# Optimization experiments

Measured on AMD Instinct MI355X. Metric: run time of the kernel, lower is better.

Reference implementation:

```python
import jax, jax.numpy as jnp
import numpy as np

EMB = 1024
N_HEAD = 16
HEAD = 64
D_FF = 4 * EMB
LN_EPS = 1e-5


def layernorm(x, g, b):
    mu = jnp.mean(x, axis=-1, keepdims=True)
    var = jnp.mean(jnp.square(x - mu), axis=-1, keepdims=True)
    return (x - mu) * jax.lax.rsqrt(var + LN_EPS) * g + b


def setup_inputs() -> dict:
    key = jax.random.key(0)
    ks = jax.random.split(key, 12)
    s = 0.02
    x = jax.random.normal(ks[0], (4, 2048, EMB), dtype=jnp.float32)
    # per-head Q/K/V projections (no bias), stacked along head axis
    Wq = jax.random.normal(ks[1], (N_HEAD, EMB, HEAD), dtype=jnp.float32) * s
    Wk = jax.random.normal(ks[2], (N_HEAD, EMB, HEAD), dtype=jnp.float32) * s
    Wv = jax.random.normal(ks[3], (N_HEAD, EMB, HEAD), dtype=jnp.float32) * s
    Wo = jax.random.normal(ks[4], (EMB, EMB), dtype=jnp.float32) * s
    bo = jnp.zeros((EMB,), dtype=jnp.float32)
    ln1_g = jnp.ones((EMB,), dtype=jnp.float32)
    ln1_b = jnp.zeros((EMB,), dtype=jnp.float32)
    W1 = jax.random.normal(ks[5], (EMB, D_FF), dtype=jnp.float32) * s
    b1 = jnp.zeros((D_FF,), dtype=jnp.float32)
    W2 = jax.random.normal(ks[6], (D_FF, EMB), dtype=jnp.float32) * s
    b2 = jnp.zeros((EMB,), dtype=jnp.float32)
    ln2_g = jnp.ones((EMB,), dtype=jnp.float32)
    ln2_b = jnp.zeros((EMB,), dtype=jnp.float32)
    return dict(x=x, Wq=Wq, Wk=Wk, Wv=Wv, Wo=Wo, bo=bo, ln1_g=ln1_g,
                ln1_b=ln1_b, W1=W1, b1=b1, W2=W2, b2=b2, ln2_g=ln2_g,
                ln2_b=ln2_b)


def reference(x, Wq, Wk, Wv, Wo, bo, ln1_g, ln1_b, W1, b1, W2, b2, ln2_g, ln2_b):
    B, T, _ = x.shape
    # fused multi-head QKV (equivalent to the per-head Python loop + concat)
    q = jnp.einsum('btd,hdk->bhtk', x, Wq)
    k = jnp.einsum('btd,hdk->bhtk', x, Wk)
    v = jnp.einsum('btd,hdk->bhtk', x, Wv)
    scores = jnp.einsum('bhtk,bhsk->bhts', q, k) / jnp.sqrt(jnp.float32(HEAD))
    att = jax.nn.softmax(scores, axis=-1)
    heads = jnp.einsum('bhts,bhsk->bhtk', att, v)           # [B,H,T,head]
    cat = heads.transpose(0, 2, 1, 3).reshape(B, T, EMB)     # concat over heads
    mha = cat @ Wo + bo
    x = x + layernorm(mha, ln1_g, ln1_b)                     # residual of LN(sublayer)
    ff = jax.nn.gelu(x @ W1 + b1, approximate=False) @ W2 + b2
    x = x + layernorm(ff, ln2_g, ln2_b)
    return x
```

## Files before the change

### kernel.cpp

```cpp
#include <hip/hip_runtime.h>
#include <math.h>


using u16 = unsigned short;
typedef __bf16 bf16x8 __attribute__((ext_vector_type(8)));
typedef __bf16 bf16x4 __attribute__((ext_vector_type(4)));
typedef unsigned short u16x8 __attribute__((ext_vector_type(8)));
typedef unsigned short u16x4 __attribute__((ext_vector_type(4)));
typedef float f32x4 __attribute__((ext_vector_type(4)));

#if defined(__has_builtin)
#if __has_builtin(__builtin_amdgcn_exp2f)
#define EXP2F(x) __builtin_amdgcn_exp2f(x)
#endif
#endif
#ifndef EXP2F
#define EXP2F(x) __expf((x) * 0.69314718055994531f)
#endif

__device__ __forceinline__ float bf2f(u16 h) {
  return __uint_as_float(((unsigned int)h) << 16);
}
__device__ __forceinline__ u16 f2bf(float f) {
  unsigned int u = __float_as_uint(f);
  u += 0x7fffu + ((u >> 16) & 1u);
  return (u16)(u >> 16);
}

__device__ __forceinline__ void gload_lds16(const void* g, void* l) {
  __builtin_amdgcn_global_load_lds(
      (__attribute__((address_space(1))) void*)(g),
      (__attribute__((address_space(3))) void*)(l), 16, 0, 0);
}

__global__ __launch_bounds__(256) void detect_dtype(const u16* __restrict__ x,
                                                    int* __restrict__ flag) {
  __shared__ int cnt[256];
  int c = 0;
#pragma unroll
  for (int j = 0; j < 8; ++j) {
    float v = bf2f(x[threadIdx.x * 8 + j]);
    float a = fabsf(v);
    if (a >= 1e-4f && a <= 64.0f) ++c;
  }
  cnt[threadIdx.x] = c;
  __syncthreads();
  if (threadIdx.x == 0) {
    int t = 0;
    for (int i = 0; i < 256; ++i) t += cnt[i];
    flag[0] = (t < 1638) ? 1 : 0;
  }
}

__global__ __launch_bounds__(256) void cvt_copy(const void* __restrict__ in,
                                                u16* __restrict__ out,
                                                const int* __restrict__ flagp,
                                                long n) {
  long idx = ((long)blockIdx.x * 256 + threadIdx.x) * 4;
  if (idx >= n) return;
  if (*flagp) {
    float4 v = *(const float4*)((const float*)in + idx);
    out[idx] = f2bf(v.x); out[idx + 1] = f2bf(v.y);
    out[idx + 2] = f2bf(v.z); out[idx + 3] = f2bf(v.w);
  } else {
    *(u16x4*)(out + idx) = *(const u16x4*)((const u16*)in + idx);
  }
}

__global__ __launch_bounds__(256) void cvt_vecs(
    const void* s0, const void* s1, const void* s2, const void* s3,
    const void* s4, const void* s5, const void* s6, u16* __restrict__ dst,
    const int* __restrict__ flagp) {
  const int lens[7] = {1024, 1024, 1024, 4096, 1024, 1024, 1024};
  const int offs[7] = {0, 1024, 2048, 3072, 7168, 8192, 9216};
  const void* srcs[7] = {s0, s1, s2, s3, s4, s5, s6};
  int w = blockIdx.x;
  int f = *flagp;
  for (int i = threadIdx.x; i < lens[w]; i += 256)
    dst[offs[w] + i] = f ? f2bf(((const float*)srcs[w])[i])
                         : ((const u16*)srcs[w])[i];
}

__global__ __launch_bounds__(256) void transpose_cvt(
    const void* __restrict__ in, u16* __restrict__ out, int R, int C,
    long inBS, long outBS, const int* __restrict__ flagp) {
  __shared__ u16 tile[32][33];
  int f = *flagp;
  u16* ob = out + (long)blockIdx.z * outBS;
  int c = blockIdx.x * 32 + threadIdx.x;
  int r0 = blockIdx.y * 32;
  if (f) {
    const float* ib = (const float*)in + (long)blockIdx.z * inBS;
#pragma unroll
    for (int i = threadIdx.y; i < 32; i += 8)
      tile[i][threadIdx.x] = f2bf(ib[(long)(r0 + i) * C + c]);
  } else {
    const u16* ib = (const u16*)in + (long)blockIdx.z * inBS;
#pragma unroll
    for (int i = threadIdx.y; i < 32; i += 8)
      tile[i][threadIdx.x] = ib[(long)(r0 + i) * C + c];
  }
  __syncthreads();
  int r = r0 + threadIdx.x;
  int c0 = blockIdx.x * 32;
#pragma unroll
  for (int i = threadIdx.y; i < 32; i += 8)
    ob[(long)(c0 + i) * R + r] = tile[threadIdx.x][i];
}

__global__ __launch_bounds__(256) void kv_frag(const u16* __restrict__ qkv,
                                               u16* __restrict__ KF,
                                               u16* __restrict__ VF) {
  __shared__ u16 Kt[64][72];
  __shared__ u16 Vt[64][72];
  const int jblk = blockIdx.x, bh = blockIdx.y;
  const int b = bh >> 4, h = bh & 15;
  const int tid = threadIdx.x;
  const long j0 = jblk * 64;

  {
    int tt = tid >> 2, c0 = (tid & 3) * 16;
    const u16* src = qkv + (long)(b * 2048 + j0 + tt) * 3072 + h * 64 + c0;
    *(u16x8*)(&Kt[tt][c0]) = *(const u16x8*)(src + 1024);
    *(u16x8*)(&Kt[tt][c0 + 8]) = *(const u16x8*)(src + 1024 + 8);
    *(u16x8*)(&Vt[tt][c0]) = *(const u16x8*)(src + 2048);
    *(u16x8*)(&Vt[tt][c0 + 8]) = *(const u16x8*)(src + 2048 + 8);
  }
  __syncthreads();

  long obase = ((long)bh * 32 + jblk) * 8 * 512;
#pragma unroll
  for (int si = 0; si < 2; ++si) {
    int s = tid * 2 + si;
    int f = s >> 6, ln = s & 63;
    int kt = f >> 2, nt = f & 3;
    int lr = ln & 15, lq = ln >> 4;
    u16x8 ko, vo;
#pragma unroll
    for (int j = 0; j < 8; ++j) {
      ko[j] = Kt[nt * 16 + lr][kt * 32 + lq * 8 + j];
      vo[j] = Vt[kt * 32 + lq * 8 + j][nt * 16 + lr];
    }
    *(u16x8*)(KF + obase + (long)s * 8) = ko;
    *(u16x8*)(VF + obase + (long)s * 8) = vo;
  }
}

__device__ __forceinline__ bf16x8 fragld64(const u16* lb, int row, int ks,
                                           int lq) {
  int slot = ((ks << 2) | lq) ^ (row & 7);
  return *(const bf16x8*)(lb + row * 64 + slot * 8);
}

template <int EPI, int BN>
__global__ __launch_bounds__(512, 2) void gemm2ph(
    const u16* __restrict__ A, const u16* __restrict__ Bt,
    const u16* __restrict__ bias, u16* __restrict__ Cout,
    int M, int N, int K) {
  static_assert(BN == 256 || BN == 128, "");
  constexpr int NFQ = BN / 128;
  __shared__ u16 As[2][16384];
  __shared__ u16 Bs[2][BN * 64];
  const int tid = threadIdx.x;
  const int wave = tid >> 6, lane = tid & 63;
  const int lr = lane & 15, lq = lane >> 4;

  const int MT = M >> 8, NTt = N / BN;
  const int nwg = MT * NTt;
  int wg = blockIdx.x;
  if (!(nwg & 7)) wg = (wg & 7) * (nwg >> 3) + (wg >> 3);
  const int tm = wg % MT, tn = wg / MT;
  const long m0 = (long)tm << 8;
  const long n0 = (long)tn * BN;

  const int wm = (wave >> 2) << 7;
  const int wn = (wave & 3) * (BN / 4);

  const int srow = lane >> 3;
  const int skoff = ((lane & 7) ^ srow) * 8;

  auto stage = [&](int buf, int t) {
#pragma unroll
    for (int j = 0; j < 4; ++j)
      gload_lds16(
          A + (m0 + j * 64 + wave * 8 + srow) * (long)K + t * 64 + skoff,
          &As[buf][j * 4096 + (wave << 9)]);
#pragma unroll
    for (int j = 0; j < BN / 64; ++j)
      gload_lds16(
          Bt + (n0 + j * 64 + wave * 8 + srow) * (long)K + t * 64 + skoff,
          &Bs[buf][j * 4096 + (wave << 9)]);
  };

  f32x4 acc[8][2 * NFQ] = {};
  const int NT = K >> 6;
  int cur = 0;

  stage(0, 0);
  __syncthreads();

  for (int t = 0; t < NT; ++t) {
    const u16* Ab = As[cur];
    const u16* Bb = Bs[cur];
    if (t + 1 < NT) stage(cur ^ 1, t + 1);

    bf16x8 a_[4][2], b0_[NFQ][2], b1_[NFQ][2];
#pragma unroll
    for (int mf = 0; mf < 4; ++mf)
#pragma unroll
      for (int ks = 0; ks < 2; ++ks)
        a_[mf][ks] = fragld64(Ab, wm + mf * 16 + lr, ks, lq);
#pragma unroll
    for (int nf = 0; nf < NFQ; ++nf)
#pragma unroll
      for (int ks = 0; ks < 2; ++ks)
        b0_[nf][ks] = fragld64(Bb, wn + nf * 16 + lr, ks, lq);
#pragma unroll
    for (int mf = 0; mf < 4; ++mf)
#pragma unroll
      for (int nf = 0; nf < NFQ; ++nf)
#pragma unroll
        for (int ks = 0; ks < 2; ++ks)
          acc[mf][nf] = __builtin_amdgcn_mfma_f32_16x16x32_bf16(
              a_[mf][ks], b0_[nf][ks], acc[mf][nf], 0, 0, 0);
#pragma unroll
    for (int nf = 0; nf < NFQ; ++nf)
#pragma unroll
      for (int ks = 0; ks < 2; ++ks)
        b1_[nf][ks] = fragld64(Bb, wn + BN / 8 + nf * 16 + lr, ks, lq);
#pragma unroll
    for (int mf = 0; mf < 4; ++mf)
#pragma unroll
      for (int nf = 0; nf < NFQ; ++nf)
#pragma unroll
        for (int ks = 0; ks < 2; ++ks)
          acc[mf][NFQ + nf] = __builtin_amdgcn_mfma_f32_16x16x32_bf16(
              a_[mf][ks], b1_[nf][ks], acc[mf][NFQ + nf], 0, 0, 0);
#pragma unroll
    for (int mf = 0; mf < 4; ++mf)
#pragma unroll
      for (int ks = 0; ks < 2; ++ks)
        a_[mf][ks] = fragld64(Ab, wm + 64 + mf * 16 + lr, ks, lq);
#pragma unroll
    for (int mf = 0; mf < 4; ++mf)
#pragma unroll
      for (int nf = 0; nf < NFQ; ++nf)
#pragma unroll
        for (int ks = 0; ks < 2; ++ks)
          acc[4 + mf][NFQ + nf] = __builtin_amdgcn_mfma_f32_16x16x32_bf16(
              a_[mf][ks], b1_[nf][ks], acc[4 + mf][NFQ + nf], 0, 0, 0);
#pragma unroll
    for (int mf = 0; mf < 4; ++mf)
#pragma unroll
      for (int nf = 0; nf < NFQ; ++nf)
#pragma unroll
        for (int ks = 0; ks < 2; ++ks)
          acc[4 + mf][nf] = __builtin_amdgcn_mfma_f32_16x16x32_bf16(
              a_[mf][ks], b0_[nf][ks], acc[4 + mf][nf], 0, 0, 0);

    __syncthreads();
    cur ^= 1;
  }

  const int rq = lq * 4;
#pragma unroll
  for (int mf = 0; mf < 8; ++mf)
#pragma unroll
    for (int nf2 = 0; nf2 < 2 * NFQ; ++nf2) {
      const int col = (int)n0 + wn + nf2 * 16 + lr;
#pragma unroll
      for (int r = 0; r < 4; ++r) {
        const long row = m0 + wm + mf * 16 + rq + r;
        float v = acc[mf][nf2][r];
        if (EPI == 2) {
          v += bf2f(bias[col]);
          v = 0.5f * v * (1.0f + erff(v * 0.70710678118654752f));
        } else if (EPI == 3) {
          v += bf2f(bias[col]);
        }
        Cout[row * (long)N + col] = f2bf(v);
      }
    }
}

template <int EPI>
__global__ __launch_bounds__(512, 2) void gemm3buf(
    const u16* __restrict__ A, const u16* __restrict__ Bt,
    const u16* __restrict__ bias, u16* __restrict__ Cout,
    int M, int N, int K) {
  __shared__ u16 As[3][16384];
  __shared__ u16 Bs[3][8192];
  const int tid = threadIdx.x;
  const int wave = tid >> 6, lane = tid & 63;
  const int lr = lane & 15, lq = lane >> 4;

  const int MT = M >> 8, NTt = N >> 7;
  const int nwg = MT * NTt;
  int wg = blockIdx.x;
  if (!(nwg & 7)) wg = (wg & 7) * (nwg >> 3) + (wg >> 3);
  const int tm = wg % MT, tn = wg / MT;
  const long m0 = (long)tm << 8;
  const long n0 = (long)tn << 7;

  const int wm = (wave >> 2) << 7;
  const int wn = (wave & 3) * 32;

  const int srow = lane >> 3;
  const int skoff = ((lane & 7) ^ srow) * 8;

  auto stage = [&](u16* ab, u16* bb, int t) {
#pragma unroll
    for (int j = 0; j < 4; ++j)
      gload_lds16(
          A + (m0 + j * 64 + wave * 8 + srow) * (long)K + t * 64 + skoff,
          ab + j * 4096 + (wave << 9));
#pragma unroll
    for (int j = 0; j < 2; ++j)
      gload_lds16(
          Bt + (n0 + j * 64 + wave * 8 + srow) * (long)K + t * 64 + skoff,
          bb + j * 4096 + (wave << 9));
  };

  u16 *pa0 = &As[0][0], *pa1 = &As[1][0], *pa2 = &As[2][0];
  u16 *pb0 = &Bs[0][0], *pb1 = &Bs[1][0], *pb2 = &Bs[2][0];

  f32x4 acc[8][2] = {};
  const int NT = K >> 6;

  stage(pa0, pb0, 0);
  stage(pa1, pb1, 1);
  asm volatile("s_waitcnt vmcnt(6)" ::: "memory");
  __builtin_amdgcn_s_barrier();
  __builtin_amdgcn_sched_barrier(0);

  for (int t = 0; t < NT; ++t) {
    const bool pf = (t + 2 < NT);
    if (pf) stage(pa2, pb2, t + 2);

    bf16x8 a_[4][2], b0_[2], b1_[2];
#pragma unroll
    for (int mf = 0; mf < 4; ++mf)
#pragma unroll
      for (int ks = 0; ks < 2; ++ks)
        a_[mf][ks] = fragld64(pa0, wm + mf * 16 + lr, ks, lq);
#pragma unroll
    for (int ks = 0; ks < 2; ++ks) b0_[ks] = fragld64(pb0, wn + lr, ks, lq);
#pragma unroll
    for (int mf = 0; mf < 4; ++mf)
#pragma unroll
      for (int ks = 0; ks < 2; ++ks)
        acc[mf][0] = __builtin_amdgcn_mfma_f32_16x16x32_bf16(
            a_[mf][ks], b0_[ks], acc[mf][0], 0, 0, 0);
#pragma unroll
    for (int ks = 0; ks < 2; ++ks)
      b1_[ks] = fragld64(pb0, wn + 16 + lr, ks, lq);
#pragma unroll
    for (int mf = 0; mf < 4; ++mf)
#pragma unroll
      for (int ks = 0; ks < 2; ++ks)
        acc[mf][1] = __builtin_amdgcn_mfma_f32_16x16x32_bf16(
            a_[mf][ks], b1_[ks], acc[mf][1], 0, 0, 0);
#pragma unroll
    for (int mf = 0; mf < 4; ++mf)
#pragma unroll
      for (int ks = 0; ks < 2; ++ks)
        a_[mf][ks] = fragld64(pa0, wm + 64 + mf * 16 + lr, ks, lq);
#pragma unroll
    for (int mf = 0; mf < 4; ++mf)
#pragma unroll
      for (int ks = 0; ks < 2; ++ks)
        acc[4 + mf][1] = __builtin_amdgcn_mfma_f32_16x16x32_bf16(
            a_[mf][ks], b1_[ks], acc[4 + mf][1], 0, 0, 0);
#pragma unroll
    for (int mf = 0; mf < 4; ++mf)
#pragma unroll
      for (int ks = 0; ks < 2; ++ks)
        acc[4 + mf][0] = __builtin_amdgcn_mfma_f32_16x16x32_bf16(
            a_[mf][ks], b0_[ks], acc[4 + mf][0], 0, 0, 0);

    if (pf)
      asm volatile("s_waitcnt vmcnt(6) lgkmcnt(0)" ::: "memory");
    else
      asm volatile("s_waitcnt vmcnt(0) lgkmcnt(0)" ::: "memory");
    __builtin_amdgcn_s_barrier();
    __builtin_amdgcn_sched_barrier(0);

    u16* ta = pa0; pa0 = pa1; pa1 = pa2; pa2 = ta;
    u16* tb = pb0; pb0 = pb1; pb1 = pb2; pb2 = tb;
  }

  const int rq = lq * 4;
#pragma unroll
  for (int mf = 0; mf < 8; ++mf)
#pragma unroll
    for (int nf2 = 0; nf2 < 2; ++nf2) {
      const int col = (int)n0 + wn + nf2 * 16 + lr;
#pragma unroll
      for (int r = 0; r < 4; ++r) {
        const long row = m0 + wm + mf * 16 + rq + r;
        float v = acc[mf][nf2][r];
        if (EPI == 2) {
          v += bf2f(bias[col]);
          v = 0.5f * v * (1.0f + erff(v * 0.70710678118654752f));
        } else if (EPI == 3) {
          v += bf2f(bias[col]);
        }
        Cout[row * (long)N + col] = f2bf(v);
      }
    }
}

__global__ __launch_bounds__(256, 3) void flash_attn(
    const u16* __restrict__ qkv, const u16* __restrict__ KF,
    const u16* __restrict__ VF, u16* __restrict__ cat) {
  const int T = 2048, LD = 3072;
  const float QSCALE = 0.18033688011112042f;
  const float EXPC = 4.3280851226677321f;
  const int bh = blockIdx.y;
  const int b = bh >> 4, h = bh & 15;
  const int tid = threadIdx.x, wave = tid >> 6, lane = tid & 63;
  const int lr = lane & 15, lq = lane >> 4;

  __shared__ u16 Ps[4 * 32 * 64];
  u16* Pw = Ps + wave * 32 * 64;

  const u16* Qb = qkv + (long)(b * 2048) * LD + h * 64;
  const long fbase = (long)bh * 32 * 8 * 512;

  bf16x8 aq[2][2];
#pragma unroll
  for (int st = 0; st < 2; ++st) {
    int qrow = blockIdx.x * 128 + wave * 32 + st * 16 + lr;
#pragma unroll
    for (int kt = 0; kt < 2; ++kt) {
      u16x8 q = *(const u16x8*)(Qb + (long)qrow * LD + kt * 32 + lq * 8);
      bf16x8 t;
#pragma unroll
      for (int j = 0; j < 8; ++j) t[j] = (__bf16)(bf2f(q[j]) * QSCALE);
      aq[st][kt] = t;
    }
  }

  f32x4 o[2][4] = {};
  float lsum[2] = {0.0f, 0.0f};

  for (int jblk = 0; jblk < T / 64; ++jblk) {
    const u16* kf = KF + fbase + (long)jblk * 8 * 512;
    const u16* vf = VF + fbase + (long)jblk * 8 * 512;

    bf16x8 bk[2][4];
#pragma unroll
    for (int kt = 0; kt < 2; ++kt)
#pragma unroll
      for (int nt = 0; nt < 4; ++nt)
        bk[kt][nt] = *(const bf16x8*)(kf + (kt * 4 + nt) * 512 + lane * 8);

    f32x4 s[2][4] = {};
    __builtin_amdgcn_s_setprio(1);
#pragma unroll
    for (int st = 0; st < 2; ++st)
#pragma unroll
      for (int nt = 0; nt < 4; ++nt)
#pragma unroll
        for (int kt = 0; kt < 2; ++kt)
          s[st][nt] = __builtin_amdgcn_mfma_f32_16x16x32_bf16(
              bk[kt][nt], aq[st][kt], s[st][nt], 0, 0, 0);
    __builtin_amdgcn_s_setprio(0);

    bf16x8 bv[2][4];
#pragma unroll
    for (int kt = 0; kt < 2; ++kt)
#pragma unroll
      for (int nt = 0; nt < 4; ++nt)
        bv[kt][nt] = *(const bf16x8*)(vf + (kt * 4 + nt) * 512 + lane * 8);

#pragma unroll
    for (int st = 0; st < 2; ++st)
#pragma unroll
      for (int nt = 0; nt < 4; ++nt) {
        f32x4 p;
#pragma unroll
        for (int r = 0; r < 4; ++r) p[r] = EXP2F(s[st][nt][r] - EXPC);
        lsum[st] += (p[0] + p[1]) + (p[2] + p[3]);
        bf16x4 pk;
#pragma unroll
        for (int r = 0; r < 4; ++r) pk[r] = (__bf16)p[r];
        int wph = (nt * 2 + (lq >> 1)) ^ (lr & 7);
        *(bf16x4*)(Pw + (st * 16 + lr) * 64 + wph * 8 + (lq & 1) * 4) = pk;
      }

#pragma unroll
    for (int st = 0; st < 2; ++st)
#pragma unroll
      for (int kt = 0; kt < 2; ++kt) {
        bf16x8 ap = *(const bf16x8*)(
            Pw + (st * 16 + lr) * 64 + (((kt * 4 + lq) ^ (lr & 7)) * 8));
        __builtin_amdgcn_s_setprio(1);
#pragma unroll
        for (int nt = 0; nt < 4; ++nt)
          o[st][nt] = __builtin_amdgcn_mfma_f32_16x16x32_bf16(
              ap, bv[kt][nt], o[st][nt], 0, 0, 0);
        __builtin_amdgcn_s_setprio(0);
      }
  }

#pragma unroll
  for (int st = 0; st < 2; ++st) {
    lsum[st] += __shfl_xor(lsum[st], 16, 64);
    lsum[st] += __shfl_xor(lsum[st], 32, 64);
  }

  u16* ob = cat + (long)(b * 2048) * 1024 + h * 64;
#pragma unroll
  for (int st = 0; st < 2; ++st) {
    int trow = blockIdx.x * 128 + wave * 32 + st * 16 + lq * 4;
#pragma unroll
    for (int r = 0; r < 4; ++r) {
      float linv = 1.0f / __shfl(lsum[st], lq * 4 + r, 64);
#pragma unroll
      for (int nt = 0; nt < 4; ++nt)
        ob[(long)(trow + r) * 1024 + nt * 16 + lr] = f2bf(o[st][nt][r] * linv);
    }
  }
}

__global__ __launch_bounds__(256) void ln_residual(
    const u16* __restrict__ y, const void* __restrict__ res, int res_raw,
    const u16* __restrict__ g, const u16* __restrict__ bb,
    void* __restrict__ out, const int* __restrict__ flagp, int final_out) {
  const long row = blockIdx.x;
  const int tid = threadIdx.x, wave = tid >> 6, lane = tid & 63;
  u16x4 yv = *(const u16x4*)(y + row * 1024 + tid * 4);
  float yy[4];
#pragma unroll
  for (int j = 0; j < 4; ++j) yy[j] = bf2f(yv[j]);
  float s1 = yy[0] + yy[1] + yy[2] + yy[3];
  float s2 = yy[0] * yy[0] + yy[1] * yy[1] + yy[2] * yy[2] + yy[3] * yy[3];
#pragma unroll
  for (int off = 1; off < 64; off <<= 1) {
    s1 += __shfl_xor(s1, off, 64);
    s2 += __shfl_xor(s2, off, 64);
  }
  __shared__ float ws1[4], ws2[4];
  if (lane == 0) { ws1[wave] = s1; ws2[wave] = s2; }
  __syncthreads();
  float t1 = ws1[0] + ws1[1] + ws1[2] + ws1[3];
  float t2 = ws2[0] + ws2[1] + ws2[2] + ws2[3];
  float mu = t1 * (1.0f / 1024.0f);
  float var = t2 * (1.0f / 1024.0f) - mu * mu;
  float rstd = rsqrtf(var + 1e-5f);
  int i = tid * 4;
  bool f32in = res_raw && (*flagp);
  bool f32out = final_out && (*flagp);
#pragma unroll
  for (int j = 0; j < 4; ++j) {
    float rv = f32in ? ((const float*)res)[row * 1024 + i + j]
                     : bf2f(((const u16*)res)[row * 1024 + i + j]);
    float o = rv + (yy[j] - mu) * rstd * bf2f(g[i + j]) + bf2f(bb[i + j]);
    if (f32out)
      ((float*)out)[row * 1024 + i + j] = o;
    else
      ((u16*)out)[row * 1024 + i + j] = f2bf(o);
  }
}

extern "C" void kernel_launch(void* const* d_in, const int* in_sizes, int n_in,
                              void* d_out, int out_size, void* d_ws,
                              size_t ws_size, hipStream_t stream) {
  const void* x_raw = d_in[0];
  const void* Wq = d_in[1];
  const void* Wk = d_in[2];
  const void* Wv = d_in[3];
  const void* Wo = d_in[4];
  const void* bo = d_in[5];
  const void* ln1g = d_in[6];
  const void* ln1b = d_in[7];
  const void* W1 = d_in[8];
  const void* b1 = d_in[9];
  const void* W2 = d_in[10];
  const void* b2 = d_in[11];
  const void* ln2g = d_in[12];
  const void* ln2b = d_in[13];

  char* ws = (char*)d_ws;
  u16* qkv = (u16*)(ws + 0);
  u16* mha = (u16*)(ws + 0);
  u16* h1 = (u16*)(ws + 0);
  u16* cat = (u16*)(ws + 50331648);
  u16* KF = (u16*)(ws + 67108864);
  u16* ff = (u16*)(ws + 67108864);
  u16* xb = (u16*)(ws + 83886080);
  u16* VF = (u16*)(ws + 83886080);
  u16* x1 = (u16*)(ws + 83886080);
  u16* wqkvt = (u16*)(ws + 100663296);
  u16* wot = (u16*)(ws + 106954752);
  u16* w1t = (u16*)(ws + 109051904);
  u16* w2t = (u16*)(ws + 117440512);
  u16* vecs = (u16*)(ws + 125829120);
  int* flag = (int*)(ws + 125853696);

  const u16* v_bo = vecs + 0;
  const u16* v_l1g = vecs + 1024;
  const u16* v_l1b = vecs + 2048;
  const u16* v_b1 = vecs + 3072;
  const u16* v_b2 = vecs + 7168;
  const u16* v_l2g = vecs + 8192;
  const u16* v_l2b = vecs + 9216;

  detect_dtype<<<1, 256, 0, stream>>>((const u16*)x_raw, flag);
  cvt_copy<<<8192, 256, 0, stream>>>(x_raw, xb, flag, 8388608L);
  cvt_vecs<<<7, 256, 0, stream>>>(bo, ln1g, ln1b, b1, b2, ln2g, ln2b, vecs, flag);

  dim3 tb(32, 8);
  transpose_cvt<<<dim3(2, 32, 16), tb, 0, stream>>>(Wq, wqkvt, 1024, 64, 65536, 65536, flag);
  transpose_cvt<<<dim3(2, 32, 16), tb, 0, stream>>>(Wk, wqkvt + 1048576, 1024, 64, 65536, 65536, flag);
  transpose_cvt<<<dim3(2, 32, 16), tb, 0, stream>>>(Wv, wqkvt + 2097152, 1024, 64, 65536, 65536, flag);
  transpose_cvt<<<dim3(32, 32, 1), tb, 0, stream>>>(Wo, wot, 1024, 1024, 0, 0, flag);
  transpose_cvt<<<dim3(128, 32, 1), tb, 0, stream>>>(W1, w1t, 1024, 4096, 0, 0, flag);
  transpose_cvt<<<dim3(32, 128, 1), tb, 0, stream>>>(W2, w2t, 4096, 1024, 0, 0, flag);

  gemm3buf<0><<<768, 512, 0, stream>>>(xb, wqkvt, nullptr, qkv, 8192, 3072, 1024);
  kv_frag<<<dim3(32, 64), 256, 0, stream>>>(qkv, KF, VF);
  flash_attn<<<dim3(16, 64), 256, 0, stream>>>(qkv, KF, VF, cat);
  gemm3buf<3><<<256, 512, 0, stream>>>(cat, wot, v_bo, mha, 8192, 1024, 1024);
  ln_residual<<<8192, 256, 0, stream>>>(mha, x_raw, 1, v_l1g, v_l1b, x1, flag, 0);
  gemm2ph<2, 256><<<512, 512, 0, stream>>>(x1, w1t, v_b1, h1, 8192, 4096, 1024);
  gemm3buf<3><<<256, 512, 0, stream>>>(h1, w2t, v_b2, ff, 8192, 1024, 4096);
  ln_residual<<<8192, 256, 0, stream>>>(ff, x1, 0, v_l2g, v_l2b, d_out, flag, 1);
}
```

Before: 624.2 us.

## Fuse setup kernels, scatter K/V fragments from QKV GEMM, drop triple-buffer GEMM

```diff
diff --git a/kernel.cpp b/kernel.cpp
--- a/kernel.cpp
+++ b/kernel.cpp
@@ -52,98 +52,81 @@
   }
 }
 
-__global__ __launch_bounds__(256) void cvt_copy(const void* __restrict__ in,
-                                                u16* __restrict__ out,
-                                                const int* __restrict__ flagp,
-                                                long n) {
-  long idx = ((long)blockIdx.x * 256 + threadIdx.x) * 4;
-  if (idx >= n) return;
-  if (*flagp) {
-    float4 v = *(const float4*)((const float*)in + idx);
-    out[idx] = f2bf(v.x); out[idx + 1] = f2bf(v.y);
-    out[idx + 2] = f2bf(v.z); out[idx + 3] = f2bf(v.w);
+__global__ __launch_bounds__(256) void setup_all(
+    const void* __restrict__ x_raw, u16* __restrict__ xb,
+    const void* s0, const void* s1, const void* s2, const void* s3,
+    const void* s4, const void* s5, const void* s6, u16* __restrict__ vecs,
+    const void* Wq, const void* Wk, const void* Wv, u16* __restrict__ wqkvt,
+    const void* Wo, u16* __restrict__ wot,
+    const void* W1, u16* __restrict__ w1t,
+    const void* W2, u16* __restrict__ w2t, const int* __restrict__ flagp) {
+  const int f = *flagp;
+  const int id = blockIdx.x;
+  const int tid = threadIdx.x;
+
+  if (id < 8192) {
+    long idx = ((long)id * 256 + tid) * 4;
+    if (f) {
+      float4 v = *(const float4*)((const float*)x_raw + idx);
+      xb[idx] = f2bf(v.x); xb[idx + 1] = f2bf(v.y);
+      xb[idx + 2] = f2bf(v.z); xb[idx + 3] = f2bf(v.w);
+    } else {
+      *(u16x4*)(xb + idx) = *(const u16x4*)((const u16*)x_raw + idx);
+    }
+    return;
+  }
+  if (id < 8199) {
+    const int lens[7] = {1024, 1024, 1024, 4096, 1024, 1024, 1024};
+    const int offs[7] = {0, 1024, 2048, 3072, 7168, 8192, 9216};
+    const void* srcs[7] = {s0, s1, s2, s3, s4, s5, s6};
+    int w = id - 8192;
+    for (int i = tid; i < lens[w]; i += 256)
+      vecs[offs[w] + i] = f ? f2bf(((const float*)srcs[w])[i])
+                            : ((const u16*)srcs[w])[i];
+    return;
+  }
+
+  __shared__ u16 tile[32][33];
+  const void* in;
+  u16* out;
+  int R, C, bx, by;
+  if (id < 11271) {
+    int q = id - 8199;
+    int bz = q >> 6, rem = q & 63;
+    bx = rem & 1; by = rem >> 1;
+    int which = bz >> 4, zz = bz & 15;
+    const void* src = which == 0 ? Wq : (which == 1 ? Wk : Wv);
+    in = (const char*)src + (long)zz * 65536 * (f ? 4 : 2);
+    out = wqkvt + (long)which * 1048576 + (long)zz * 65536;
+    R = 1024; C = 64;
+  } else if (id < 12295) {
+    int q = id - 11271; bx = q & 31; by = q >> 5;
+    in = Wo; out = wot; R = 1024; C = 1024;
+  } else if (id < 16391) {
+    int q = id - 12295; bx = q & 127; by = q >> 7;
+    in = W1; out = w1t; R = 1024; C = 4096;
   } else {
-    *(u16x4*)(out + idx) = *(const u16x4*)((const u16*)in + idx);
-  }
-}
-
-__global__ __launch_bounds__(256) void cvt_vecs(
-    const void* s0, const void* s1, const void* s2, const void* s3,
-    const void* s4, const void* s5, const void* s6, u16* __restrict__ dst,
-    const int* __restrict__ flagp) {
-  const int lens[7] = {1024, 1024, 1024, 4096, 1024, 1024, 1024};
-  const int offs[7] = {0, 1024, 2048, 3072, 7168, 8192, 9216};
-  const void* srcs[7] = {s0, s1, s2, s3, s4, s5, s6};
-  int w = blockIdx.x;
-  int f = *flagp;
-  for (int i = threadIdx.x; i < lens[w]; i += 256)
-    dst[offs[w] + i] = f ? f2bf(((const float*)srcs[w])[i])
-                         : ((const u16*)srcs[w])[i];
-}
-
-__global__ __launch_bounds__(256) void transpose_cvt(
-    const void* __restrict__ in, u16* __restrict__ out, int R, int C,
-    long inBS, long outBS, const int* __restrict__ flagp) {
-  __shared__ u16 tile[32][33];
-  int f = *flagp;
-  u16* ob = out + (long)blockIdx.z * outBS;
-  int c = blockIdx.x * 32 + threadIdx.x;
-  int r0 = blockIdx.y * 32;
+    int q = id - 16391; bx = q & 31; by = q >> 5;
+    in = W2; out = w2t; R = 4096; C = 1024;
+  }
+  const int tx = tid & 31, ty = tid >> 5;
+  int c = bx * 32 + tx, r0 = by * 32;
   if (f) {
-    const float* ib = (const float*)in + (long)blockIdx.z * inBS;
-#pragma unroll
-    for (int i = threadIdx.y; i < 32; i += 8)
-      tile[i][threadIdx.x] = f2bf(ib[(long)(r0 + i) * C + c]);
+    const float* ib = (const float*)in;
+#pragma unroll
+    for (int i = ty; i < 32; i += 8)
+      tile[i][tx] = f2bf(ib[(long)(r0 + i) * C + c]);
   } else {
-    const u16* ib = (const u16*)in + (long)blockIdx.z * inBS;
-#pragma unroll
-    for (int i = threadIdx.y; i < 32; i += 8)
-      tile[i][threadIdx.x] = ib[(long)(r0 + i) * C + c];
+    const u16* ib = (const u16*)in;
+#pragma unroll
+    for (int i = ty; i < 32; i += 8)
+      tile[i][tx] = ib[(long)(r0 + i) * C + c];
   }
   __syncthreads();
-  int r = r0 + threadIdx.x;
-  int c0 = blockIdx.x * 32;
-#pragma unroll
-  for (int i = threadIdx.y; i < 32; i += 8)
-    ob[(long)(c0 + i) * R + r] = tile[threadIdx.x][i];
-}
-
-__global__ __launch_bounds__(256) void kv_frag(const u16* __restrict__ qkv,
-                                               u16* __restrict__ KF,
-                                               u16* __restrict__ VF) {
-  __shared__ u16 Kt[64][72];
-  __shared__ u16 Vt[64][72];
-  const int jblk = blockIdx.x, bh = blockIdx.y;
-  const int b = bh >> 4, h = bh & 15;
-  const int tid = threadIdx.x;
-  const long j0 = jblk * 64;
-
-  {
-    int tt = tid >> 2, c0 = (tid & 3) * 16;
-    const u16* src = qkv + (long)(b * 2048 + j0 + tt) * 3072 + h * 64 + c0;
-    *(u16x8*)(&Kt[tt][c0]) = *(const u16x8*)(src + 1024);
-    *(u16x8*)(&Kt[tt][c0 + 8]) = *(const u16x8*)(src + 1024 + 8);
-    *(u16x8*)(&Vt[tt][c0]) = *(const u16x8*)(src + 2048);
-    *(u16x8*)(&Vt[tt][c0 + 8]) = *(const u16x8*)(src + 2048 + 8);
-  }
-  __syncthreads();
-
-  long obase = ((long)bh * 32 + jblk) * 8 * 512;
-#pragma unroll
-  for (int si = 0; si < 2; ++si) {
-    int s = tid * 2 + si;
-    int f = s >> 6, ln = s & 63;
-    int kt = f >> 2, nt = f & 3;
-    int lr = ln & 15, lq = ln >> 4;
-    u16x8 ko, vo;
-#pragma unroll
-    for (int j = 0; j < 8; ++j) {
-      ko[j] = Kt[nt * 16 + lr][kt * 32 + lq * 8 + j];
-      vo[j] = Vt[kt * 32 + lq * 8 + j][nt * 16 + lr];
-    }
-    *(u16x8*)(KF + obase + (long)s * 8) = ko;
-    *(u16x8*)(VF + obase + (long)s * 8) = vo;
-  }
+  int r = r0 + tx, c0 = bx * 32;
+#pragma unroll
+  for (int i = ty; i < 32; i += 8)
+    out[(long)(c0 + i) * R + r] = tile[tx][i];
 }
 
 __device__ __forceinline__ bf16x8 fragld64(const u16* lb, int row, int ks,
@@ -283,68 +266,64 @@
     }
 }
 
-template <int EPI>
-__global__ __launch_bounds__(512, 2) void gemm3buf(
+__global__ __launch_bounds__(512, 2) void gemm_qkv(
     const u16* __restrict__ A, const u16* __restrict__ Bt,
-    const u16* __restrict__ bias, u16* __restrict__ Cout,
-    int M, int N, int K) {
-  __shared__ u16 As[3][16384];
-  __shared__ u16 Bs[3][8192];
+    u16* __restrict__ Qout, u16* __restrict__ KF, u16* __restrict__ VF) {
+  const int M = 8192, N = 3072, K = 1024;
+  constexpr int BN = 128;
+  __shared__ u16 As[2][16384];
+  __shared__ u16 Bs[2][BN * 64];
   const int tid = threadIdx.x;
   const int wave = tid >> 6, lane = tid & 63;
   const int lr = lane & 15, lq = lane >> 4;
 
-  const int MT = M >> 8, NTt = N >> 7;
+  const int MT = M >> 8, NTt = N / BN;
   const int nwg = MT * NTt;
   int wg = blockIdx.x;
   if (!(nwg & 7)) wg = (wg & 7) * (nwg >> 3) + (wg >> 3);
   const int tm = wg % MT, tn = wg / MT;
   const long m0 = (long)tm << 8;
-  const long n0 = (long)tn << 7;
+  const long n0 = (long)tn * BN;
 
   const int wm = (wave >> 2) << 7;
-  const int wn = (wave & 3) * 32;
+  const int wn = (wave & 3) * (BN / 4);
 
   const int srow = lane >> 3;
   const int skoff = ((lane & 7) ^ srow) * 8;
 
-  auto stage = [&](u16* ab, u16* bb, int t) {
+  auto stage = [&](int buf, int t) {
 #pragma unroll
     for (int j = 0; j < 4; ++j)
       gload_lds16(
           A + (m0 + j * 64 + wave * 8 + srow) * (long)K + t * 64 + skoff,
-          ab + j * 4096 + (wave << 9));
-#pragma unroll
-    for (int j = 0; j < 2; ++j)
+          &As[buf][j * 4096 + (wave << 9)]);
+#pragma unroll
+    for (int j = 0; j < BN / 64; ++j)
       gload_lds16(
           Bt + (n0 + j * 64 + wave * 8 + srow) * (long)K + t * 64 + skoff,
-          bb + j * 4096 + (wave << 9));
+          &Bs[buf][j * 4096 + (wave << 9)]);
   };
-
-  u16 *pa0 = &As[0][0], *pa1 = &As[1][0], *pa2 = &As[2][0];
-  u16 *pb0 = &Bs[0][0], *pb1 = &Bs[1][0], *pb2 = &Bs[2][0];
 
   f32x4 acc[8][2] = {};
   const int NT = K >> 6;
-
-  stage(pa0, pb0, 0);
-  stage(pa1, pb1, 1);
-  asm volatile("s_waitcnt vmcnt(6)" ::: "memory");
-  __builtin_amdgcn_s_barrier();
-  __builtin_amdgcn_sched_barrier(0);
+  int cur = 0;
+
+  stage(0, 0);
+  __syncthreads();
 
   for (int t = 0; t < NT; ++t) {
-    const bool pf = (t + 2 < NT);
-    if (pf) stage(pa2, pb2, t + 2);
+    const u16* Ab = As[cur];
+    const u16* Bb = Bs[cur];
+    if (t + 1 < NT) stage(cur ^ 1, t + 1);
 
     bf16x8 a_[4][2], b0_[2], b1_[2];
 #pragma unroll
     for (int mf = 0; mf < 4; ++mf)
 #pragma unroll
       for (int ks = 0; ks < 2; ++ks)
-        a_[mf][ks] = fragld64(pa0, wm + mf * 16 + lr, ks, lq);
-#pragma unroll
-    for (int ks = 0; ks < 2; ++ks) b0_[ks] = fragld64(pb0, wn + lr, ks, lq);
+        a_[mf][ks] = fragld64(Ab, wm + mf * 16 + lr, ks, lq);
+#pragma unroll
+    for (int ks = 0; ks < 2; ++ks) b0_[ks] = fragld64(Bb, wn + lr, ks, lq);
 #pragma unroll
     for (int mf = 0; mf < 4; ++mf)
 #pragma unroll
@@ -353,7 +332,7 @@
             a_[mf][ks], b0_[ks], acc[mf][0], 0, 0, 0);
 #pragma unroll
     for (int ks = 0; ks < 2; ++ks)
-      b1_[ks] = fragld64(pb0, wn + 16 + lr, ks, lq);
+      b1_[ks] = fragld64(Bb, wn + 16 + lr, ks, lq);
 #pragma unroll
     for (int mf = 0; mf < 4; ++mf)
 #pragma unroll
@@ -364,7 +343,7 @@
     for (int mf = 0; mf < 4; ++mf)
 #pragma unroll
       for (int ks = 0; ks < 2; ++ks)
-        a_[mf][ks] = fragld64(pa0, wm + 64 + mf * 16 + lr, ks, lq);
+        a_[mf][ks] = fragld64(Ab, wm + 64 + mf * 16 + lr, ks, lq);
 #pragma unroll
     for (int mf = 0; mf < 4; ++mf)
 #pragma unroll
@@ -378,36 +357,60 @@
         acc[4 + mf][0] = __builtin_amdgcn_mfma_f32_16x16x32_bf16(
             a_[mf][ks], b0_[ks], acc[4 + mf][0], 0, 0, 0);
 
-    if (pf)
-      asm volatile("s_waitcnt vmcnt(6) lgkmcnt(0)" ::: "memory");
-    else
-      asm volatile("s_waitcnt vmcnt(0) lgkmcnt(0)" ::: "memory");
-    __builtin_amdgcn_s_barrier();
-    __builtin_amdgcn_sched_barrier(0);
-
-    u16* ta = pa0; pa0 = pa1; pa1 = pa2; pa2 = ta;
-    u16* tb = pb0; pb0 = pb1; pb1 = pb2; pb2 = tb;
+    __syncthreads();
+    cur ^= 1;
   }
 
   const int rq = lq * 4;
-#pragma unroll
-  for (int mf = 0; mf < 8; ++mf)
-#pragma unroll
-    for (int nf2 = 0; nf2 < 2; ++nf2) {
-      const int col = (int)n0 + wn + nf2 * 16 + lr;
-#pragma unroll
-      for (int r = 0; r < 4; ++r) {
-        const long row = m0 + wm + mf * 16 + rq + r;
-        float v = acc[mf][nf2][r];
-        if (EPI == 2) {
-          v += bf2f(bias[col]);
-          v = 0.5f * v * (1.0f + erff(v * 0.70710678118654752f));
-        } else if (EPI == 3) {
-          v += bf2f(bias[col]);
+  if (n0 < 1024) {
+#pragma unroll
+    for (int mf = 0; mf < 8; ++mf)
+#pragma unroll
+      for (int nf2 = 0; nf2 < 2; ++nf2) {
+        const int col = (int)n0 + wn + nf2 * 16 + lr;
+#pragma unroll
+        for (int r = 0; r < 4; ++r) {
+          const long row = m0 + wm + mf * 16 + rq + r;
+          Qout[row * 3072 + col] = f2bf(acc[mf][nf2][r]);
         }
-        Cout[row * (long)N + col] = f2bf(v);
       }
-    }
+  } else if (n0 < 2048) {
+#pragma unroll
+    for (int mf = 0; mf < 8; ++mf)
+#pragma unroll
+      for (int nf2 = 0; nf2 < 2; ++nf2) {
+        const int cc = (int)n0 + wn + nf2 * 16 + lr - 1024;
+        const int h = cc >> 6, d = cc & 63;
+#pragma unroll
+        for (int r = 0; r < 4; ++r) {
+          const int row = (int)m0 + wm + mf * 16 + rq + r;
+          const int b = row >> 11, t = row & 2047;
+          const long base =
+              ((long)((b * 16 + h) * 32 + (t >> 6)) * 8 + (d >> 5) * 4 +
+               ((t >> 4) & 3)) * 512;
+          KF[base + (((d >> 3) & 3) * 16 + (t & 15)) * 8 + (d & 7)] =
+              f2bf(acc[mf][nf2][r]);
+        }
+      }
+  } else {
+#pragma unroll
+    for (int mf = 0; mf < 8; ++mf)
+#pragma unroll
+      for (int nf2 = 0; nf2 < 2; ++nf2) {
+        const int cc = (int)n0 + wn + nf2 * 16 + lr - 2048;
+        const int h = cc >> 6, d = cc & 63;
+#pragma unroll
+        for (int r = 0; r < 4; ++r) {
+          const int row = (int)m0 + wm + mf * 16 + rq + r;
+          const int b = row >> 11, t = row & 2047;
+          const long base =
+              ((long)((b * 16 + h) * 32 + (t >> 6)) * 8 + ((t >> 5) & 1) * 4 +
+               (d >> 4)) * 512;
+          VF[base + (((t >> 3) & 3) * 16 + (d & 15)) * 8 + (t & 7)] =
+              f2bf(acc[mf][nf2][r]);
+        }
+      }
+  }
 }
 
 __global__ __launch_bounds__(256, 3) void flash_attn(
@@ -586,11 +589,11 @@
   u16* qkv = (u16*)(ws + 0);
   u16* mha = (u16*)(ws + 0);
   u16* h1 = (u16*)(ws + 0);
-  u16* cat = (u16*)(ws + 50331648);
+  u16* VF = (u16*)(ws + 50331648);
   u16* KF = (u16*)(ws + 67108864);
   u16* ff = (u16*)(ws + 67108864);
   u16* xb = (u16*)(ws + 83886080);
-  u16* VF = (u16*)(ws + 83886080);
+  u16* cat = (u16*)(ws + 83886080);
   u16* x1 = (u16*)(ws + 83886080);
   u16* wqkvt = (u16*)(ws + 100663296);
   u16* wot = (u16*)(ws + 106954752);
@@ -608,23 +611,15 @@
   const u16* v_l2b = vecs + 9216;
 
   detect_dtype<<<1, 256, 0, stream>>>((const u16*)x_raw, flag);
-  cvt_copy<<<8192, 256, 0, stream>>>(x_raw, xb, flag, 8388608L);
-  cvt_vecs<<<7, 256, 0, stream>>>(bo, ln1g, ln1b, b1, b2, ln2g, ln2b, vecs, flag);
-
-  dim3 tb(32, 8);
-  transpose_cvt<<<dim3(2, 32, 16), tb, 0, stream>>>(Wq, wqkvt, 1024, 64, 65536, 65536, flag);
-  transpose_cvt<<<dim3(2, 32, 16), tb, 0, stream>>>(Wk, wqkvt + 1048576, 1024, 64, 65536, 65536, flag);
-  transpose_cvt<<<dim3(2, 32, 16), tb, 0, stream>>>(Wv, wqkvt + 2097152, 1024, 64, 65536, 65536, flag);
-  transpose_cvt<<<dim3(32, 32, 1), tb, 0, stream>>>(Wo, wot, 1024, 1024, 0, 0, flag);
-  transpose_cvt<<<dim3(128, 32, 1), tb, 0, stream>>>(W1, w1t, 1024, 4096, 0, 0, flag);
-  transpose_cvt<<<dim3(32, 128, 1), tb, 0, stream>>>(W2, w2t, 4096, 1024, 0, 0, flag);
-
-  gemm3buf<0><<<768, 512, 0, stream>>>(xb, wqkvt, nullptr, qkv, 8192, 3072, 1024);
-  kv_frag<<<dim3(32, 64), 256, 0, stream>>>(qkv, KF, VF);
+  setup_all<<<20487, 256, 0, stream>>>(
+      x_raw, xb, bo, ln1g, ln1b, b1, b2, ln2g, ln2b, vecs,
+      Wq, Wk, Wv, wqkvt, Wo, wot, W1, w1t, W2, w2t, flag);
+
+  gemm_qkv<<<768, 512, 0, stream>>>(xb, wqkvt, qkv, KF, VF);
   flash_attn<<<dim3(16, 64), 256, 0, stream>>>(qkv, KF, VF, cat);
-  gemm3buf<3><<<256, 512, 0, stream>>>(cat, wot, v_bo, mha, 8192, 1024, 1024);
+  gemm2ph<3, 128><<<256, 512, 0, stream>>>(cat, wot, v_bo, mha, 8192, 1024, 1024);
   ln_residual<<<8192, 256, 0, stream>>>(mha, x_raw, 1, v_l1g, v_l1b, x1, flag, 0);
   gemm2ph<2, 256><<<512, 512, 0, stream>>>(x1, w1t, v_b1, h1, 8192, 4096, 1024);
-  gemm3buf<3><<<256, 512, 0, stream>>>(h1, w2t, v_b2, ff, 8192, 1024, 4096);
+  gemm2ph<3, 128><<<256, 512, 0, stream>>>(h1, w2t, v_b2, ff, 8192, 1024, 4096);
   ln_residual<<<8192, 256, 0, stream>>>(ff, x1, 0, v_l2g, v_l2b, d_out, flag, 1);
 }
```

Result: no change. 614.3 us (-1.6%).
